# Optimization experiments

Measured on AMD Instinct MI355X. Metric: run time of the kernel, lower is better.

## Reference

```python
import jax, jax.numpy as jnp
import numpy as np
import math

D_MODEL = 1024
NUM_HEADS = 16
HEAD_DIM = D_MODEL // NUM_HEADS
BATCH = 2
SEQ = 2048
NEG_INF = -1000000.0  # matches torch code's -1e6 fill


def setup_inputs() -> dict:
    key = jax.random.key(0)
    ks = jax.random.split(key, 10)
    s = 1.0 / math.sqrt(D_MODEL)
    inp = {
        "X": jax.random.normal(ks[0], (BATCH, SEQ, D_MODEL), dtype=jnp.float32),
        "Wq": jax.random.uniform(ks[1], (D_MODEL, D_MODEL), minval=-s, maxval=s, dtype=jnp.float32),
        "bq": jnp.zeros((D_MODEL,), jnp.float32),
        "Wk": jax.random.uniform(ks[2], (D_MODEL, D_MODEL), minval=-s, maxval=s, dtype=jnp.float32),
        "bk": jnp.zeros((D_MODEL,), jnp.float32),
        "Wv": jax.random.uniform(ks[3], (D_MODEL, D_MODEL), minval=-s, maxval=s, dtype=jnp.float32),
        "bv": jnp.zeros((D_MODEL,), jnp.float32),
        "Wo": jax.random.uniform(ks[4], (D_MODEL, D_MODEL), minval=-s, maxval=s, dtype=jnp.float32),
        "bo": jnp.zeros((D_MODEL,), jnp.float32),
        "valid_lens": jax.random.randint(ks[5], (BATCH, NUM_HEADS), 1, SEQ + 1, dtype=jnp.int64)
        if jax.config.jax_enable_x64 else
        jax.random.randint(ks[5], (BATCH, NUM_HEADS), 1, SEQ + 1, dtype=jnp.int32),
    }
    return inp


def _split_heads(Y, B, S):
    # (B, S, D) -> (B*H, S, head_dim), matching transpose_qkv
    return Y.reshape(B, S, NUM_HEADS, HEAD_DIM).transpose(0, 2, 1, 3).reshape(B * NUM_HEADS, S, HEAD_DIM)


def reference(X, Wq, bq, Wk, bk, Wv, bv, Wo, bo, valid_lens):
    B, S, D = X.shape
    q = _split_heads(X @ Wq.T + bq, B, S)
    k = _split_heads(X @ Wk.T + bk, B, S)
    v = _split_heads(X @ Wv.T + bv, B, S)
    scores = jnp.einsum("bqd,bkd->bqk", q, k) / math.sqrt(HEAD_DIM)  # (B*H, S, S)
    # Faithful to torch code: 2-D valid_lens reshaped to (B*H,), mask over
    # the first two dims -> entire query rows j >= valid_len set to -1e6.
    row_mask = jnp.arange(S)[None, :] < valid_lens.reshape(-1)[:, None]  # (B*H, S)
    scores = jnp.where(row_mask[:, :, None], scores, NEG_INF)
    attn = jax.nn.softmax(scores, axis=-1)
    out = jnp.einsum("bqk,bkd->bqd", attn, v)  # (B*H, S, head_dim)
    out = out.reshape(B, NUM_HEADS, S, HEAD_DIM).transpose(0, 2, 1, 3).reshape(B, S, D)
    return out @ Wo.T + bo
```

## Files before the change

### kernel.cpp

```cpp
#include <hip/hip_runtime.h>

#define SQ 2048
#define DM 1024
#define NH 16
#define HD 64

typedef __bf16 bf16x8 __attribute__((ext_vector_type(8)));
typedef float f32x4 __attribute__((ext_vector_type(4)));
typedef unsigned short u16;
typedef unsigned int u32;

__device__ __forceinline__ u16 f2b(float f) {
  union { float f; u32 u; } c; c.f = f;
  return (u16)((c.u + 0x7FFFu + ((c.u >> 16) & 1u)) >> 16);
}

__device__ __forceinline__ void gll16(const void* g, void* l) {
  __builtin_amdgcn_global_load_lds(
      (const __attribute__((address_space(1))) void*)g,
      (__attribute__((address_space(3))) void*)l, 16, 0, 0);
}

__global__ void __launch_bounds__(256) conv_bf16(
    const float* __restrict__ X,
    const float* __restrict__ Wq, const float* __restrict__ Wk,
    const float* __restrict__ Wv, const float* __restrict__ Wo,
    u16* __restrict__ Xb, u16* __restrict__ Wqb, u16* __restrict__ Wkb,
    u16* __restrict__ Wvb, u16* __restrict__ Wob) {
  const size_t e = ((size_t)blockIdx.x * 256 + threadIdx.x) * 8;
  const float* src; u16* dst; size_t rel;
  if (e < 4194304u)      { src = X;  dst = Xb;  rel = e; }
  else if (e < 5242880u) { src = Wq; dst = Wqb; rel = e - 4194304u; }
  else if (e < 6291456u) { src = Wk; dst = Wkb; rel = e - 5242880u; }
  else if (e < 7340032u) { src = Wv; dst = Wvb; rel = e - 6291456u; }
  else                   { src = Wo; dst = Wob; rel = e - 7340032u; }
  float4 a = *(const float4*)(src + rel);
  float4 b = *(const float4*)(src + rel + 4);
  union { u16 h[8]; uint4 v; } o;
  o.h[0] = f2b(a.x); o.h[1] = f2b(a.y); o.h[2] = f2b(a.z); o.h[3] = f2b(a.w);
  o.h[4] = f2b(b.x); o.h[5] = f2b(b.y); o.h[6] = f2b(b.z); o.h[7] = f2b(b.w);
  *(uint4*)(dst + rel) = o.v;
}

__global__ void __launch_bounds__(256) mean_v(
    const u16* __restrict__ Vt, u16* __restrict__ mv) {
  __shared__ float part[256];
  const int bh = blockIdx.x;
  const int t = threadIdx.x, d = t >> 2, c = t & 3;
  const u16* row = Vt + ((size_t)bh * HD + d) * SQ + c * 512;
  float s = 0.f;
  for (int i = 0; i < 64; ++i) {
    bf16x8 v = *(const bf16x8*)(row + i * 8);
    s += ((float)v[0] + (float)v[1]) + ((float)v[2] + (float)v[3])
       + ((float)v[4] + (float)v[5]) + ((float)v[6] + (float)v[7]);
  }
  part[t] = s;
  __syncthreads();
  if (c == 0) {
    const float tot = (part[t] + part[t + 1]) + (part[t + 2] + part[t + 3]);
    mv[bh * HD + d] = f2b(tot * (1.0f / 2048.0f));
  }
}

__global__ void __launch_bounds__(64) build_wl(const int* __restrict__ vlen,
                                               int* __restrict__ wl) {
  __shared__ int nts[32];
  __shared__ int off[32];
  const int t = threadIdx.x;
  int nt = 0;
  if (t < 32) {
    const int vl = vlen[t];
    nt = (vl + 63) >> 6;
    if (nt > 32) nt = 32;
    nts[t] = nt;
  }
  __syncthreads();
  if (t == 0) {
    int acc = 0;
    for (int i = 0; i < 32; ++i) { off[i] = acc; acc += nts[i]; }
    wl[0] = acc;
  }
  __syncthreads();
  if (t < 32) {
    const int o = off[t];
    for (int q = 0; q < nt; ++q) wl[1 + o + q] = (t << 5) | q;
  }
}

__global__ void __launch_bounds__(256) fill_masked(
    const int* __restrict__ vlen, const u16* __restrict__ mv, u16* __restrict__ Ao) {
  const int bh = blockIdx.x, qt = blockIdx.y;
  if (qt * 64 < vlen[bh]) return;
  const int t = threadIdx.x, w = t >> 6, l = t & 63, lg = l >> 4, li = l & 15;
  const int b = bh >> 4, h = bh & 15;
  const size_t rowb = ((size_t)(b * SQ + qt * 64 + w * 16 + li)) * DM + h * HD;
#pragma unroll
  for (int n2 = 0; n2 < 4; ++n2) {
    const uint2 v = *(const uint2*)(mv + bh * HD + n2 * 16 + lg * 4);
    *(uint2*)(Ao + rowb + n2 * 16 + lg * 4) = v;
  }
}

__global__ void __launch_bounds__(256, 3) qkv_gemm(
    const u16* __restrict__ Xb, const u16* __restrict__ Wqkv,
    const float* __restrict__ bq, const float* __restrict__ bk, const float* __restrict__ bv,
    const int* __restrict__ vlen,
    u16* __restrict__ Qb, u16* __restrict__ Kb, u16* __restrict__ Vt) {
  __shared__ u16 sA[3][4096];
  __shared__ u16 sB[3][4096];
  const int id = blockIdx.x;
  const int swz = (id & 7) * 96 + (id >> 3);
  const int bx = swz % 24, by = swz / 24;
  const int m0 = by * 128, n0 = bx * 128;
  const int mode = n0 >> 10;
  const float* bias = (mode == 0) ? bq : (mode == 1) ? bk : bv;

  if (mode == 0) {
    const int bb = m0 >> 11, s0 = m0 & 2047, h0 = n0 >> 6;
    if (s0 >= vlen[bb * NH + h0] && s0 >= vlen[bb * NH + h0 + 1]) return;
  }

  const int t = threadIdx.x, l = t & 63, w = t >> 6;
  const int wr = w >> 1, wc = w & 1, lg = l >> 4, li = l & 15;

  int srcOff[2];
#pragma unroll
  for (int j = 0; j < 2; ++j) {
    const int g = w * 2 + j;
    const int row = g * 16 + (l >> 2);
    const int colsrc = ((l & 3) * 8) ^ (((row >> 3) & 1) << 4);
    srcOff[j] = row * DM + colsrc;
  }
  const u16* Abase = Xb + (size_t)m0 * DM;
  const u16* Bbase = Wqkv + (size_t)n0 * DM;

  auto stage = [&](int buf, int kt) {
#pragma unroll
    for (int j = 0; j < 2; ++j) {
      gll16(Abase + srcOff[j] + kt * 32, &sA[buf][(w * 2 + j) * 512]);
      gll16(Bbase + srcOff[j] + kt * 32, &sB[buf][(w * 2 + j) * 512]);
    }
  };

  f32x4 acc[4][4];
  f32x4 z4 = {0.f, 0.f, 0.f, 0.f};
#pragma unroll
  for (int i = 0; i < 4; ++i)
#pragma unroll
    for (int j = 0; j < 4; ++j) acc[i][j] = z4;

  stage(0, 0);
  stage(1, 1);
  for (int kt = 0; kt < 32; ++kt) {
    const int bsel = kt % 3;
    if (kt + 2 < 32) stage((kt + 2) % 3, kt + 2);
    if (kt < 30)      asm volatile("s_waitcnt vmcnt(8)" ::: "memory");
    else if (kt == 30) asm volatile("s_waitcnt vmcnt(4)" ::: "memory");
    else               asm volatile("s_waitcnt vmcnt(0)" ::: "memory");
    __builtin_amdgcn_s_barrier();
    asm volatile("" ::: "memory");

    bf16x8 aF[4], bF[4];
#pragma unroll
    for (int mi = 0; mi < 4; ++mi) {
      const int rl = wr * 64 + mi * 16 + li;
      aF[mi] = *(const bf16x8*)(&sA[bsel][rl * 32 + ((lg * 8) ^ (((rl >> 3) & 1) << 4))]);
    }
#pragma unroll
    for (int ni = 0; ni < 4; ++ni) {
      const int rn = wc * 64 + ni * 16 + li;
      bF[ni] = *(const bf16x8*)(&sB[bsel][rn * 32 + ((lg * 8) ^ (((rn >> 3) & 1) << 4))]);
    }
    __builtin_amdgcn_s_setprio(1);
#pragma unroll
    for (int mi = 0; mi < 4; ++mi)
#pragma unroll
      for (int ni = 0; ni < 4; ++ni)
        acc[mi][ni] = __builtin_amdgcn_mfma_f32_16x16x32_bf16(aF[mi], bF[ni], acc[mi][ni], 0, 0, 0);
    __builtin_amdgcn_s_setprio(0);
    asm volatile("" ::: "memory");
    __builtin_amdgcn_s_barrier();
    asm volatile("" ::: "memory");
  }

#pragma unroll
  for (int mi = 0; mi < 4; ++mi) {
    const int m = m0 + wr * 64 + mi * 16 + lg * 4;
    const int b = m >> 11;
    const int s = m & 2047;
#pragma unroll
    for (int ni = 0; ni < 4; ++ni) {
      const int n = n0 + wc * 64 + ni * 16 + li;
      const int nn = n - (mode << 10);
      const int h = nn >> 6, dd = nn & 63;
      const float bia = bias[nn];
      const size_t bh = (size_t)(b * NH + h);
      if (mode == 2) {
        union { u16 h4[4]; uint2 u; } pk;
#pragma unroll
        for (int r = 0; r < 4; ++r) pk.h4[r] = f2b(acc[mi][ni][r] + bia);
        *(uint2*)(Vt + (bh * HD + dd) * SQ + s) = pk.u;
      } else {
#pragma unroll
        for (int r = 0; r < 4; ++r) {
          const float val = acc[mi][ni][r] + bia;
          const int ss = s + r;
          if (mode == 0) Qb[(bh * SQ + ss) * HD + dd] = f2b(val * 0.180336880f);
          else           Kb[(bh * SQ + ss) * HD + dd] = f2b(val);
        }
      }
    }
  }
}

__global__ void __launch_bounds__(256) out_gemm(
    const u16* __restrict__ Ag, const u16* __restrict__ Wob,
    const float* __restrict__ bo, float* __restrict__ out) {
  __shared__ u16 sA[2][2048];
  __shared__ u16 sB[2][4096];
  const int t = threadIdx.x, l = t & 63, w = t >> 6;
  const int wr = w >> 1, wc = w & 1, lg = l >> 4, li = l & 15;
  const int m0 = blockIdx.y * 64, n0 = blockIdx.x * 128;

  auto stage = [&](int buf, int kt) {
    {
      const int s = w * 64 + l;
      const int r = s >> 2, cc = s & 3;
      gll16(Ag + (size_t)(m0 + r) * DM + kt * 32 + cc * 8, &sA[buf][w * 512]);
    }
#pragma unroll
    for (int c = 0; c < 2; ++c) {
      const int g = w * 2 + c;
      const int s = g * 64 + l;
      const int r = s >> 2, cc = s & 3;
      gll16(Wob + (size_t)(n0 + r) * DM + kt * 32 + cc * 8, &sB[buf][g * 512]);
    }
  };

  f32x4 acc[2][4];
  f32x4 z4 = {0.f, 0.f, 0.f, 0.f};
#pragma unroll
  for (int i = 0; i < 2; ++i)
#pragma unroll
    for (int j = 0; j < 4; ++j) acc[i][j] = z4;

  stage(0, 0);
  __syncthreads();
  int cur = 0;
  for (int kt = 0; kt < DM / 32; ++kt) {
    if (kt + 1 < DM / 32) stage(cur ^ 1, kt + 1);
    bf16x8 aF[2], bF[4];
#pragma unroll
    for (int mi = 0; mi < 2; ++mi)
      aF[mi] = *(const bf16x8*)(&sA[cur][(wr * 32 + mi * 16 + li) * 32 + lg * 8]);
#pragma unroll
    for (int ni = 0; ni < 4; ++ni)
      bF[ni] = *(const bf16x8*)(&sB[cur][(wc * 64 + ni * 16 + li) * 32 + lg * 8]);
#pragma unroll
    for (int mi = 0; mi < 2; ++mi)
#pragma unroll
      for (int ni = 0; ni < 4; ++ni)
        acc[mi][ni] = __builtin_amdgcn_mfma_f32_16x16x32_bf16(aF[mi], bF[ni], acc[mi][ni], 0, 0, 0);
    __syncthreads();
    cur ^= 1;
  }

#pragma unroll
  for (int mi = 0; mi < 2; ++mi) {
    const int m = m0 + wr * 32 + mi * 16 + lg * 4;
#pragma unroll
    for (int ni = 0; ni < 4; ++ni) {
      const int n = n0 + wc * 64 + ni * 16 + li;
      const float bia = bo[n];
#pragma unroll
      for (int r = 0; r < 4; ++r)
        out[(size_t)(m + r) * DM + n] = acc[mi][ni][r] + bia;
    }
  }
}

__global__ void __launch_bounds__(256, 2) attn_v13(
    const u16* __restrict__ Qb, const u16* __restrict__ Kb, const u16* __restrict__ Vt,
    const int* __restrict__ vlen, const int* __restrict__ wl, u16* __restrict__ Ao) {
  __shared__ u16 sKV[4][10240];
  const int t = threadIdx.x, w = t >> 6, l = t & 63, lg = l >> 4, li = l & 15;
  const int nit = wl[0];

  int kOff[4], vOff[4];
#pragma unroll
  for (int i = 0; i < 4; ++i) {
    {
      const int s = i * 64 + l, row = s >> 3, c = s & 7;
      const int csrc = c ^ (row & 7);
      const int sig = (((row >> 2) & 3) << 3) | (((row >> 4) & 1) << 2) | (row & 3);
      kOff[i] = sig * HD + csrc * 8;
    }
    {
      const int s = i * 64 + l, d = s >> 2, c = s & 3;
      const int csrc = c ^ ((d >> 2) & 3);
      vOff[i] = d * SQ + csrc * 8;
    }
  }

  union { u16 h[8]; bf16x8 v; } onesU;
#pragma unroll
  for (int j = 0; j < 8; ++j) onesU.h[j] = 0x3F80;
  const bf16x8 ones = onesU.v;

  u16* sw = &sKV[w][0];
  f32x4* op = (f32x4*)&sKV[0][0];
  float* lp = (float*)((char*)&sKV[0][0] + 65536);

  for (int it = blockIdx.x; it < nit; it += gridDim.x) {
    const int item = wl[1 + it];
    const int bh = item >> 5, qt = item & 31;
    const int vl = vlen[bh];
    const int q0 = qt * 64;
    const int b = bh >> 4, h = bh & 15;
    const u16* Qh = Qb + (size_t)bh * SQ * HD;
    const u16* Kh = Kb + (size_t)bh * SQ * HD;
    const u16* Vh = Vt + (size_t)bh * HD * SQ;
    const int k0 = w * 512;

    bf16x8 qf[4][2];
#pragma unroll
    for (int g = 0; g < 4; ++g) {
      const bool mq = (q0 + g * 16 + li) >= vl;
#pragma unroll
      for (int kk = 0; kk < 2; ++kk) {
        qf[g][kk] = *(const bf16x8*)(Qh + (size_t)(q0 + g * 16 + li) * HD + kk * 32 + lg * 8);
        if (mq) {
          union { u32 u[4]; bf16x8 v; } z; z.u[0] = z.u[1] = z.u[2] = z.u[3] = 0;
          qf[g][kk] = z.v;
        }
      }
    }

    auto stageK = [&](int buf, int tt) {
      const u16* kb = Kh + (size_t)(k0 + tt * 32) * HD;
#pragma unroll
      for (int i = 0; i < 4; ++i) gll16(kb + kOff[i], sw + buf * 2048 + i * 512);
    };
    auto stageV = [&](int buf, int tt) {
      const u16* vb = Vh + (size_t)(k0 + tt * 32);
#pragma unroll
      for (int i = 0; i < 4; ++i) gll16(vb + vOff[i], sw + 6144 + buf * 2048 + i * 512);
    };

    f32x4 z4 = {0.f, 0.f, 0.f, 0.f};
    f32x4 acc[4][4], lacc[4];
#pragma unroll
    for (int g = 0; g < 4; ++g) {
      lacc[g] = z4;
#pragma unroll
      for (int n2 = 0; n2 < 4; ++n2) acc[g][n2] = z4;
    }

    stageV(0, 0); stageK(0, 0); stageK(1, 1);
    for (int tt = 0; tt < 16; ++tt) {
      if (tt + 1 < 16) stageV((tt + 1) & 1, tt + 1);
      if (tt + 2 < 16) stageK((tt + 2) % 3, tt + 2);
      if (tt <= 13)      asm volatile("s_waitcnt vmcnt(12)" ::: "memory");
      else if (tt == 14) asm volatile("s_waitcnt vmcnt(8)" ::: "memory");
      else               asm volatile("s_waitcnt vmcnt(0)" ::: "memory");
      const u16* kb_ = sw + (tt % 3) * 2048;
      const u16* vb_ = sw + 6144 + (tt & 1) * 2048;

      bf16x8 kf[2][2], vf[4];
#pragma unroll
      for (int ni = 0; ni < 2; ++ni) {
        const int row = ni * 16 + li;
        kf[ni][0] = *(const bf16x8*)(kb_ + row * 64 + ((lg ^ (row & 7)) * 8));
        kf[ni][1] = *(const bf16x8*)(kb_ + row * 64 + (((4 + lg) ^ (row & 7)) * 8));
      }
#pragma unroll
      for (int n2 = 0; n2 < 4; ++n2) {
        const int d = n2 * 16 + li;
        vf[n2] = *(const bf16x8*)(vb_ + d * 32 + ((lg ^ ((d >> 2) & 3)) * 8));
      }

      __builtin_amdgcn_s_setprio(1);
#pragma unroll
      for (int g = 0; g < 4; ++g) {
        f32x4 s0 = __builtin_amdgcn_mfma_f32_16x16x32_bf16(kf[0][0], qf[g][0], z4, 0, 0, 0);
        s0 = __builtin_amdgcn_mfma_f32_16x16x32_bf16(kf[0][1], qf[g][1], s0, 0, 0, 0);
        f32x4 s1 = __builtin_amdgcn_mfma_f32_16x16x32_bf16(kf[1][0], qf[g][0], z4, 0, 0, 0);
        s1 = __builtin_amdgcn_mfma_f32_16x16x32_bf16(kf[1][1], qf[g][1], s1, 0, 0, 0);

        union { __bf16 e[8]; bf16x8 v; } P;
#pragma unroll
        for (int r = 0; r < 4; ++r) {
          P.e[r]     = (__bf16)__builtin_amdgcn_exp2f(s0[r]);
          P.e[4 + r] = (__bf16)__builtin_amdgcn_exp2f(s1[r]);
        }

        lacc[g] = __builtin_amdgcn_mfma_f32_16x16x32_bf16(ones, P.v, lacc[g], 0, 0, 0);
#pragma unroll
        for (int n2 = 0; n2 < 4; ++n2)
          acc[g][n2] = __builtin_amdgcn_mfma_f32_16x16x32_bf16(vf[n2], P.v, acc[g][n2], 0, 0, 0);
      }
      __builtin_amdgcn_s_setprio(0);
    }

    __syncthreads();
#pragma unroll
    for (int g = 0; g < 4; ++g) {
#pragma unroll
      for (int n2 = 0; n2 < 4; ++n2)
        op[(((w * 4) + g) * 4 + n2) * 64 + l] = acc[g][n2];
      if (lg == 0) lp[(w * 4 + g) * 16 + li] = lacc[g][0];
    }
    __syncthreads();

    const int g = w;
    const float lf = lp[(0 * 4 + g) * 16 + li] + lp[(1 * 4 + g) * 16 + li]
                   + lp[(2 * 4 + g) * 16 + li] + lp[(3 * 4 + g) * 16 + li];
    const float inv = 1.0f / lf;
    const size_t rowb = ((size_t)(b * SQ + q0 + g * 16 + li)) * DM + h * HD;
#pragma unroll
    for (int n2 = 0; n2 < 4; ++n2) {
      f32x4 s = op[((0 * 4 + g) * 4 + n2) * 64 + l];
      s += op[((1 * 4 + g) * 4 + n2) * 64 + l];
      s += op[((2 * 4 + g) * 4 + n2) * 64 + l];
      s += op[((3 * 4 + g) * 4 + n2) * 64 + l];
      union { __bf16 h2[4]; uint2 u; } ov;
#pragma unroll
      for (int r = 0; r < 4; ++r) ov.h2[r] = (__bf16)(s[r] * inv);
      *(uint2*)(Ao + rowb + n2 * 16 + lg * 4) = ov.u;
    }
    __syncthreads();
  }
}

extern "C" void kernel_launch(void* const* d_in, const int* in_sizes, int n_in,
                              void* d_out, int out_size, void* d_ws, size_t ws_size,
                              hipStream_t stream) {
  const float* X  = (const float*)d_in[0];
  const float* Wq = (const float*)d_in[1];
  const float* bq = (const float*)d_in[2];
  const float* Wk = (const float*)d_in[3];
  const float* bk = (const float*)d_in[4];
  const float* Wv = (const float*)d_in[5];
  const float* bv = (const float*)d_in[6];
  const float* Wo = (const float*)d_in[7];
  const float* bo = (const float*)d_in[8];
  const int* vlen = (const int*)d_in[9];

  char* ws = (char*)d_ws;
  u16* Qb  = (u16*)(ws);
  u16* Kb  = (u16*)(ws + (size_t)8388608);
  u16* Vt  = (u16*)(ws + (size_t)16777216);
  u16* Xb  = (u16*)(ws + (size_t)25165824);
  u16* Ao  = Xb;
  u16* Wqb = (u16*)(ws + (size_t)33554432);
  u16* Wkb = (u16*)(ws + (size_t)35651584);
  u16* Wvb = (u16*)(ws + (size_t)37748736);
  u16* Wob = (u16*)(ws + (size_t)39845888);

  u16* mv = (u16*)d_out;
  int* wl = (int*)((char*)d_out + 8192);

  dim3 blk(256);
  conv_bf16<<<4096, blk, 0, stream>>>(X, Wq, Wk, Wv, Wo, Xb, Wqb, Wkb, Wvb, Wob);
  build_wl<<<1, 64, 0, stream>>>(vlen, wl);
  qkv_gemm<<<768, blk, 0, stream>>>(Xb, Wqb, bq, bk, bv, vlen, Qb, Kb, Vt);
  mean_v<<<32, blk, 0, stream>>>(Vt, mv);
  fill_masked<<<dim3(32, 32), blk, 0, stream>>>(vlen, mv, Ao);
  attn_v13<<<512, blk, 0, stream>>>(Qb, Kb, Vt, vlen, wl, Ao);
  out_gemm<<<dim3(8, 64), blk, 0, stream>>>(Ao, Wob, bo, (float*)d_out);
}
```

Measured before the change: 121.6 us.

## Fuse mean, masked-row fill and worklist build; batch QK MFMAs before exp

New measurement: 118.2 us. 1.03x faster.

```diff
diff --git a/kernel.cpp b/kernel.cpp
--- a/kernel.cpp
+++ b/kernel.cpp
@@ -42,9 +42,11 @@
   *(uint4*)(dst + rel) = o.v;
 }
 
-__global__ void __launch_bounds__(256) mean_v(
-    const u16* __restrict__ Vt, u16* __restrict__ mv) {
+__global__ void __launch_bounds__(256) mean_v2(
+    const u16* __restrict__ Vt, const int* __restrict__ vlen,
+    u16* __restrict__ Ao, int* __restrict__ wl) {
   __shared__ float part[256];
+  __shared__ float smv[64];
   const int bh = blockIdx.x;
   const int t = threadIdx.x, d = t >> 2, c = t & 3;
   const u16* row = Vt + ((size_t)bh * HD + d) * SQ + c * 512;
@@ -58,46 +60,38 @@
   __syncthreads();
   if (c == 0) {
     const float tot = (part[t] + part[t + 1]) + (part[t + 2] + part[t + 3]);
-    mv[bh * HD + d] = f2b(tot * (1.0f / 2048.0f));
-  }
-}
-
-__global__ void __launch_bounds__(64) build_wl(const int* __restrict__ vlen,
-                                               int* __restrict__ wl) {
-  __shared__ int nts[32];
-  __shared__ int off[32];
-  const int t = threadIdx.x;
-  int nt = 0;
-  if (t < 32) {
-    const int vl = vlen[t];
-    nt = (vl + 63) >> 6;
-    if (nt > 32) nt = 32;
-    nts[t] = nt;
+    smv[d] = tot * (1.0f / 2048.0f);
   }
   __syncthreads();
-  if (t == 0) {
-    int acc = 0;
-    for (int i = 0; i < 32; ++i) { off[i] = acc; acc += nts[i]; }
-    wl[0] = acc;
-  }
-  __syncthreads();
-  if (t < 32) {
-    const int o = off[t];
-    for (int q = 0; q < nt; ++q) wl[1 + o + q] = (t << 5) | q;
-  }
-}
-
-__global__ void __launch_bounds__(256) fill_masked(
-    const int* __restrict__ vlen, const u16* __restrict__ mv, u16* __restrict__ Ao) {
-  const int bh = blockIdx.x, qt = blockIdx.y;
-  if (qt * 64 < vlen[bh]) return;
-  const int t = threadIdx.x, w = t >> 6, l = t & 63, lg = l >> 4, li = l & 15;
+
+  const int vl = vlen[bh];
+  const int ft = (vl + 63) >> 6;
   const int b = bh >> 4, h = bh & 15;
-  const size_t rowb = ((size_t)(b * SQ + qt * 64 + w * 16 + li)) * DM + h * HD;
-#pragma unroll
-  for (int n2 = 0; n2 < 4; ++n2) {
-    const uint2 v = *(const uint2*)(mv + bh * HD + n2 * 16 + lg * 4);
-    *(uint2*)(Ao + rowb + n2 * 16 + lg * 4) = v;
+  const int c16 = t & 15, r16 = t >> 4;
+  union { u16 h4[4]; uint2 u; } pv;
+#pragma unroll
+  for (int j = 0; j < 4; ++j) pv.h4[j] = f2b(smv[c16 * 4 + j]);
+  for (int ss = ft * 64 + r16; ss < SQ; ss += 16)
+    *(uint2*)(Ao + ((size_t)(b * SQ + ss)) * DM + h * HD + c16 * 4) = pv.u;
+
+  if (bh == 0) {
+    __shared__ int nts[32], off[32];
+    if (t < 32) {
+      int nt = (vlen[t] + 63) >> 6;
+      if (nt > 32) nt = 32;
+      nts[t] = nt;
+    }
+    __syncthreads();
+    if (t == 0) {
+      int acc = 0;
+      for (int i = 0; i < 32; ++i) { off[i] = acc; acc += nts[i]; }
+      wl[0] = acc;
+    }
+    __syncthreads();
+    if (t < 32) {
+      const int o = off[t], nt = nts[t];
+      for (int q = 0; q < nt; ++q) wl[1 + o + q] = (t << 5) | q;
+    }
   }
 }
 
@@ -279,7 +273,7 @@
   }
 }
 
-__global__ void __launch_bounds__(256, 2) attn_v13(
+__global__ void __launch_bounds__(256, 2) attn_v14(
     const u16* __restrict__ Qb, const u16* __restrict__ Kb, const u16* __restrict__ Vt,
     const int* __restrict__ vlen, const int* __restrict__ wl, u16* __restrict__ Ao) {
   __shared__ u16 sKV[4][10240];
@@ -379,25 +373,39 @@
         vf[n2] = *(const bf16x8*)(vb_ + d * 32 + ((lg ^ ((d >> 2) & 3)) * 8));
       }
 
+      f32x4 s0a[4], s1a[4];
       __builtin_amdgcn_s_setprio(1);
 #pragma unroll
       for (int g = 0; g < 4; ++g) {
-        f32x4 s0 = __builtin_amdgcn_mfma_f32_16x16x32_bf16(kf[0][0], qf[g][0], z4, 0, 0, 0);
-        s0 = __builtin_amdgcn_mfma_f32_16x16x32_bf16(kf[0][1], qf[g][1], s0, 0, 0, 0);
-        f32x4 s1 = __builtin_amdgcn_mfma_f32_16x16x32_bf16(kf[1][0], qf[g][0], z4, 0, 0, 0);
-        s1 = __builtin_amdgcn_mfma_f32_16x16x32_bf16(kf[1][1], qf[g][1], s1, 0, 0, 0);
-
+        s0a[g] = __builtin_amdgcn_mfma_f32_16x16x32_bf16(kf[0][0], qf[g][0], z4, 0, 0, 0);
+        s1a[g] = __builtin_amdgcn_mfma_f32_16x16x32_bf16(kf[1][0], qf[g][0], z4, 0, 0, 0);
+      }
+#pragma unroll
+      for (int g = 0; g < 4; ++g) {
+        s0a[g] = __builtin_amdgcn_mfma_f32_16x16x32_bf16(kf[0][1], qf[g][1], s0a[g], 0, 0, 0);
+        s1a[g] = __builtin_amdgcn_mfma_f32_16x16x32_bf16(kf[1][1], qf[g][1], s1a[g], 0, 0, 0);
+      }
+      __builtin_amdgcn_s_setprio(0);
+
+      bf16x8 Pv[4];
+#pragma unroll
+      for (int g = 0; g < 4; ++g) {
         union { __bf16 e[8]; bf16x8 v; } P;
 #pragma unroll
         for (int r = 0; r < 4; ++r) {
-          P.e[r]     = (__bf16)__builtin_amdgcn_exp2f(s0[r]);
-          P.e[4 + r] = (__bf16)__builtin_amdgcn_exp2f(s1[r]);
+          P.e[r]     = (__bf16)__builtin_amdgcn_exp2f(s0a[g][r]);
+          P.e[4 + r] = (__bf16)__builtin_amdgcn_exp2f(s1a[g][r]);
         }
-
-        lacc[g] = __builtin_amdgcn_mfma_f32_16x16x32_bf16(ones, P.v, lacc[g], 0, 0, 0);
+        Pv[g] = P.v;
+      }
+
+      __builtin_amdgcn_s_setprio(1);
+#pragma unroll
+      for (int g = 0; g < 4; ++g) {
+        lacc[g] = __builtin_amdgcn_mfma_f32_16x16x32_bf16(ones, Pv[g], lacc[g], 0, 0, 0);
 #pragma unroll
         for (int n2 = 0; n2 < 4; ++n2)
-          acc[g][n2] = __builtin_amdgcn_mfma_f32_16x16x32_bf16(vf[n2], P.v, acc[g][n2], 0, 0, 0);
+          acc[g][n2] = __builtin_amdgcn_mfma_f32_16x16x32_bf16(vf[n2], Pv[g], acc[g][n2], 0, 0, 0);
       }
       __builtin_amdgcn_s_setprio(0);
     }
@@ -457,15 +465,12 @@
   u16* Wvb = (u16*)(ws + (size_t)37748736);
   u16* Wob = (u16*)(ws + (size_t)39845888);
 
-  u16* mv = (u16*)d_out;
   int* wl = (int*)((char*)d_out + 8192);
 
   dim3 blk(256);
   conv_bf16<<<4096, blk, 0, stream>>>(X, Wq, Wk, Wv, Wo, Xb, Wqb, Wkb, Wvb, Wob);
-  build_wl<<<1, 64, 0, stream>>>(vlen, wl);
   qkv_gemm<<<768, blk, 0, stream>>>(Xb, Wqb, bq, bk, bv, vlen, Qb, Kb, Vt);
-  mean_v<<<32, blk, 0, stream>>>(Vt, mv);
-  fill_masked<<<dim3(32, 32), blk, 0, stream>>>(vlen, mv, Ao);
-  attn_v13<<<512, blk, 0, stream>>>(Qb, Kb, Vt, vlen, wl, Ao);
+  mean_v2<<<32, blk, 0, stream>>>(Vt, vlen, Ao, wl);
+  attn_v14<<<512, blk, 0, stream>>>(Qb, Kb, Vt, vlen, wl, Ao);
   out_gemm<<<dim3(8, 64), blk, 0, stream>>>(Ao, Wob, bo, (float*)d_out);
 }
```
